# Kernel tuning notes

Hardware: AMD Instinct MI355X
Metric: run time of the kernel (lower is better)

The kernel has to match this reference:

```python
import jax, jax.numpy as jnp
import numpy as np


def setup_inputs() -> dict:
    key = jax.random.key(0)
    ks = jax.random.split(key, 9)
    B, Cin, H, W = 16, 512, 64, 64
    Cout = 256
    s_in = 0.02  # small init scale for stable softmax
    return {
        "x": jax.random.normal(ks[0], (B, Cin, H, W), dtype=jnp.float32),
        "Wq": jax.random.normal(ks[1], (Cout, Cin), dtype=jnp.float32) * s_in,
        "bq": jnp.zeros((Cout,), dtype=jnp.float32),
        "Wk": jax.random.normal(ks[2], (Cout, Cin), dtype=jnp.float32) * s_in,
        "bk": jnp.zeros((Cout,), dtype=jnp.float32),
        "Wv": jax.random.normal(ks[3], (Cout, Cin), dtype=jnp.float32) * s_in,
        "bv": jnp.zeros((Cout,), dtype=jnp.float32),
        "Wo": jax.random.normal(ks[4], (Cin, Cout), dtype=jnp.float32) * s_in,
        "bo": jnp.zeros((Cin,), dtype=jnp.float32),
    }


def reference(x, Wq, bq, Wk, bk, Wv, bv, Wo, bo):
    B, C, H, W = x.shape
    N = H * W
    xf = x.reshape(B, C, N)  # flatten spatial
    # 1x1 convs == per-pixel linear maps over channels
    q = jnp.einsum('oc,bcn->bon', Wq, xf) + bq[None, :, None]  # [B,Cout,N]
    k = jnp.einsum('oc,bcn->bon', Wk, xf) + bk[None, :, None]
    v = jnp.einsum('oc,bcn->bon', Wv, xf) + bv[None, :, None]
    # NOTE: original contracts over spatial dim N -> channel-attention [B,Cout,Cout]
    scale = jnp.asarray(N, x.dtype) ** 0.5  # query.size(-1) == N
    scores = jnp.einsum('bcn,bdn->bcd', q, k) / scale
    attn = jax.nn.softmax(scores, axis=-1)  # softmax over key-channel dim
    out = jnp.einsum('bcd,bdn->bcn', attn, v)  # [B,Cout,N]
    # permute(0,2,1).view(B,-1,H,W): row-major reshape of (B,N,Cout)
    out = jnp.transpose(out, (0, 2, 1)).reshape(B, -1, H, W)  # [B,Cout,H,W]
    out = jnp.einsum('co,bohw->bchw', Wo, out) + bo[None, :, None, None]
    return out
```

## Files before the change

### kernel.cpp

```cpp
#include <hip/hip_runtime.h>
#include <math.h>

typedef unsigned short u16;
typedef __bf16 bf16x8 __attribute__((ext_vector_type(8)));
typedef float f32x4 __attribute__((ext_vector_type(4)));
typedef unsigned short u16x4 __attribute__((ext_vector_type(4)));
typedef unsigned short u16x8 __attribute__((ext_vector_type(8)));

__device__ __forceinline__ u16 f2bf(float f) {
    unsigned int u = __float_as_uint(f);
    return (u16)((u + 0x7FFF + ((u >> 16) & 1)) >> 16);
}

#define BAR() do { __builtin_amdgcn_sched_barrier(0); __builtin_amdgcn_s_barrier(); __builtin_amdgcn_sched_barrier(0); } while (0)

__device__ __forceinline__ void stg(
    const u16* __restrict__ g, int ld, int row0, int rstride, int kt,
    u16* lds, int w, int l)
{
    #pragma unroll
    for (int qq = 0; qq < 2; ++qq) {
        const int c0 = qq * 512 + w * 64;
        const int c  = c0 + l;
        const int row = c & 255, kc = c >> 8;
        const u16* src = g + (size_t)(row0 + row * rstride) * ld + kt + kc * 8;
        __builtin_amdgcn_global_load_lds(
            (const __attribute__((address_space(1))) unsigned int*)src,
            (__attribute__((address_space(3))) unsigned int*)(lds + (size_t)c0 * 8),
            16, 0, 0);
    }
}

template<int NT>
__device__ __forceinline__ void gemm256(
    const u16* __restrict__ Ag, int ldA, int baseA, int rsA,
    const u16* __restrict__ Bg, int ldB, int n0,
    u16* sm, f32x4 (&acc)[8][4])
{
    const int tid = threadIdx.x;
    const int l = tid & 63, w = tid >> 6;
    const int p = l & 15, g = l >> 4;
    const int wm = (w >> 2) * 128;
    const int wn = (w & 3) * 64;

    #pragma unroll
    for (int t = 0; t < 3; ++t) {
        u16* buf = sm + (t & 3) * 16384;
        stg(Ag, ldA, baseA, rsA, t * 32, buf, w, l);
        stg(Bg, ldB, n0, 1, t * 32, buf + 8192, w, l);
    }

    #pragma unroll
    for (int t = 0; t < NT; ++t) {
        u16* bufA = sm + (t & 3) * 16384;
        u16* bufB = bufA + 8192;
        u16* nbuf = sm + ((t + 3) & 3) * 16384;

        if (t + 3 < NT) stg(Ag, ldA, baseA, rsA, (t + 3) * 32, nbuf, w, l);
        {
            const int r = NT - 1 - t;
            if (r >= 3)      asm volatile("s_waitcnt vmcnt(10)" ::: "memory");
            else if (r == 2) asm volatile("s_waitcnt vmcnt(8)"  ::: "memory");
            else if (r == 1) asm volatile("s_waitcnt vmcnt(4)"  ::: "memory");
            else             asm volatile("s_waitcnt vmcnt(0)"  ::: "memory");
        }
        BAR();
        bf16x8 bfr[4];
        #pragma unroll
        for (int nf = 0; nf < 4; ++nf) {
            int row = wn + nf * 16 + p;
            bfr[nf] = *(const bf16x8*)(bufB + (size_t)(g * 256 + row) * 8);
        }
        {
            bf16x8 af[4];
            #pragma unroll
            for (int i = 0; i < 4; ++i) {
                int row = wm + i * 16 + p;
                af[i] = *(const bf16x8*)(bufA + (size_t)(g * 256 + row) * 8);
            }
            __builtin_amdgcn_s_setprio(1);
            #pragma unroll
            for (int i = 0; i < 4; ++i)
                #pragma unroll
                for (int nf = 0; nf < 4; ++nf)
                    acc[i][nf] = __builtin_amdgcn_mfma_f32_16x16x32_bf16(af[i], bfr[nf], acc[i][nf], 0, 0, 0);
            __builtin_amdgcn_s_setprio(0);
        }
        if (t + 3 < NT) stg(Bg, ldB, n0, 1, (t + 3) * 32, nbuf + 8192, w, l);
        {
            bf16x8 af[4];
            #pragma unroll
            for (int i = 0; i < 4; ++i) {
                int row = wm + (4 + i) * 16 + p;
                af[i] = *(const bf16x8*)(bufA + (size_t)(g * 256 + row) * 8);
            }
            __builtin_amdgcn_s_setprio(1);
            #pragma unroll
            for (int i = 0; i < 4; ++i)
                #pragma unroll
                for (int nf = 0; nf < 4; ++nf)
                    acc[4 + i][nf] = __builtin_amdgcn_mfma_f32_16x16x32_bf16(af[i], bfr[nf], acc[4 + i][nf], 0, 0, 0);
            __builtin_amdgcn_s_setprio(0);
        }
        BAR();
    }
}

__global__ __launch_bounds__(256) void k0_prep(
    const float* __restrict__ x, u16* __restrict__ xT,
    const float* __restrict__ Wq, const float* __restrict__ Wk,
    const float* __restrict__ Wv, const float* __restrict__ Wo,
    u16* __restrict__ wqk, u16* __restrict__ wv, u16* __restrict__ wo)
{
    const int tid = threadIdx.x;
    if (blockIdx.z == 16) {
        const int bid = blockIdx.y * 64 + blockIdx.x;
        const int sel = bid >> 7;
        const int sub = bid & 127;
        const float* s = sel == 0 ? Wq : sel == 1 ? Wk : sel == 2 ? Wv : Wo;
        u16* d = sel == 0 ? wqk : sel == 1 ? (wqk + 131072) : sel == 2 ? wv : wo;
        int i = (sub * 256 + tid) * 4;
        float4 v = *(const float4*)(s + i);
        u16x4 u = {f2bf(v.x), f2bf(v.y), f2bf(v.z), f2bf(v.w)};
        *(u16x4*)(d + i) = u;
        return;
    }
    __shared__ float Tx[64 * 65];
    const int b = blockIdx.z, c0 = blockIdx.y * 64, n0 = blockIdx.x * 64;
    const float* xb = x + (size_t)b * 512 * 4096;
    #pragma unroll
    for (int r = 0; r < 4; ++r) {
        int crow = (tid >> 4) + r * 16;
        int ncol = (tid & 15) * 4;
        float4 v = *(const float4*)(xb + (size_t)(c0 + crow) * 4096 + n0 + ncol);
        Tx[(ncol + 0) * 65 + crow] = v.x;
        Tx[(ncol + 1) * 65 + crow] = v.y;
        Tx[(ncol + 2) * 65 + crow] = v.z;
        Tx[(ncol + 3) * 65 + crow] = v.w;
    }
    __syncthreads();
    u16* ob = xT + (size_t)b * 4096 * 512;
    #pragma unroll
    for (int cc = 0; cc < 2; ++cc) {
        int id = cc * 256 + tid;
        int nrow = id >> 3;
        int cch = (id & 7) * 8;
        u16x8 u;
        #pragma unroll
        for (int j = 0; j < 8; ++j) u[j] = f2bf(Tx[nrow * 65 + cch + j]);
        *(u16x8*)(ob + (size_t)(n0 + nrow) * 512 + c0 + cch) = u;
    }
}

__global__ __launch_bounds__(512, 2) void k1_qkv(
    const u16* __restrict__ wqk, const u16* __restrict__ wv,
    const float* __restrict__ bq, const float* __restrict__ bk, const float* __restrict__ bv,
    const u16* __restrict__ xT, u16* __restrict__ q, u16* __restrict__ kmat,
    u16* __restrict__ vT)
{
    __shared__ u16 sm[65536];
    const int b = blockIdx.z;
    const int y = blockIdx.y;
    const u16* xb = xT + (size_t)b * 4096 * 512;

    const int tid = threadIdx.x;
    const int l = tid & 63, w = tid >> 6;
    const int p = l & 15, g = l >> 4;
    const int wm = (w >> 2) * 128, wn = (w & 3) * 64;

    f32x4 acc[8][4] = {};

    if (y < 2) {
        const int m0 = y * 256;
        const int n0 = blockIdx.x * 256;
        gemm256<16>(wqk, 512, m0, 1, xb, 512, n0, sm, acc);

        const float* bias = (y == 0) ? bq : bk;
        u16* outp = ((y == 0) ? q : kmat) + ((size_t)b << 20);
        #pragma unroll
        for (int mf = 0; mf < 8; ++mf)
            #pragma unroll
            for (int nf = 0; nf < 4; ++nf) {
                int n = n0 + wn + nf * 16 + p;
                #pragma unroll
                for (int r = 0; r < 4; ++r) {
                    int mloc = wm + mf * 16 + g * 4 + r;
                    outp[(size_t)mloc * 4096 + n] = f2bf(acc[mf][nf][r] + bias[mloc]);
                }
            }
    } else {
        const int m0 = blockIdx.x * 256;
        gemm256<16>(xb, 512, m0, 1, wv, 512, 0, sm, acc);

        u16* outp = vT + ((size_t)b << 20);
        #pragma unroll
        for (int nf = 0; nf < 4; ++nf) {
            int d = wn + nf * 16 + p;
            float bvv = bv[d];
            #pragma unroll
            for (int mf = 0; mf < 8; ++mf) {
                #pragma unroll
                for (int r = 0; r < 4; ++r) {
                    int row = m0 + wm + mf * 16 + g * 4 + r;
                    outp[(size_t)row * 256 + d] = f2bf(acc[mf][nf][r] + bvv);
                }
            }
        }
    }
}

__global__ __launch_bounds__(512, 2) void k2_scores(
    const u16* __restrict__ q, const u16* __restrict__ kmat, float* __restrict__ spart)
{
    __shared__ u16 sm[65536];
    const int b = blockIdx.z;
    const int split = blockIdx.x;
    const u16* A = q    + ((size_t)b << 20) + split * 512;
    const u16* B = kmat + ((size_t)b << 20) + split * 512;

    f32x4 acc[8][4] = {};
    gemm256<16>(A, 4096, 0, 1, B, 4096, 0, sm, acc);

    const int tid = threadIdx.x;
    const int l = tid & 63, w = tid >> 6;
    const int p = l & 15, g = l >> 4;
    const int wm = (w >> 2) * 128, wn = (w & 3) * 64;

    float* sp = spart + ((size_t)split * 16 + b) * 65536;
    #pragma unroll
    for (int mf = 0; mf < 8; ++mf)
        #pragma unroll
        for (int nf = 0; nf < 4; ++nf) {
            int n = wn + nf * 16 + p;
            #pragma unroll
            for (int r = 0; r < 4; ++r) {
                int m = wm + mf * 16 + g * 4 + r;
                sp[(size_t)m * 256 + n] = acc[mf][nf][r] * 0.015625f;
            }
        }
}

__global__ __launch_bounds__(256) void k3_softmax(
    const float* __restrict__ sp, u16* __restrict__ attn)
{
    const int row = blockIdx.x;
    const int tid = threadIdx.x;
    const size_t STRIDE = (size_t)16 * 65536;
    const size_t base = (size_t)row * 256 + tid;

    float s = 0.f;
    #pragma unroll
    for (int i = 0; i < 8; ++i) s += sp[base + i * STRIDE];

    __shared__ float red[4];
    float m = s;
    #pragma unroll
    for (int off = 32; off >= 1; off >>= 1) m = fmaxf(m, __shfl_xor(m, off));
    if ((tid & 63) == 0) red[tid >> 6] = m;
    __syncthreads();
    m = fmaxf(fmaxf(red[0], red[1]), fmaxf(red[2], red[3]));

    float e = expf(s - m);
    float t = e;
    #pragma unroll
    for (int off = 32; off >= 1; off >>= 1) t += __shfl_xor(t, off);
    __syncthreads();
    if ((tid & 63) == 0) red[tid >> 6] = t;
    __syncthreads();
    t = red[0] + red[1] + red[2] + red[3];

    attn[base] = f2bf(e / t);
}

__global__ __launch_bounds__(512, 2) void k4_pv(
    const u16* __restrict__ attn, const u16* __restrict__ vT, u16* __restrict__ outT3)
{
    __shared__ u16 sm[65536];
    const int b  = blockIdx.z;
    const int sh = blockIdx.x;
    const u16* A = vT   + ((size_t)b << 20);
    const u16* B = attn + ((size_t)b << 16);

    f32x4 acc[8][4] = {};
    gemm256<8>(A, 256, sh, 16, B, 256, 0, sm, acc);

    const int tid = threadIdx.x;
    const int l = tid & 63, w = tid >> 6;
    const int p = l & 15, g = l >> 4;
    const int wm = (w >> 2) * 128, wn = (w & 3) * 64;

    u16* outp = outT3 + (((size_t)b * 16 + sh) << 16);
    #pragma unroll
    for (int mf = 0; mf < 8; ++mf)
        #pragma unroll
        for (int nf = 0; nf < 4; ++nf) {
            int co  = wn + nf * 16 + p;
            int nh0 = wm + mf * 16 + g * 4;
            u16x4 u = {f2bf(acc[mf][nf][0]), f2bf(acc[mf][nf][1]),
                       f2bf(acc[mf][nf][2]), f2bf(acc[mf][nf][3])};
            *(u16x4*)(outp + (size_t)co * 256 + nh0) = u;
        }
}

__global__ __launch_bounds__(512, 2) void k5_final(
    const u16* __restrict__ wo, const float* __restrict__ bo,
    const u16* __restrict__ outT3, float* __restrict__ out)
{
    __shared__ u16 sm[65536];
    const int bz = blockIdx.z;
    const int b  = bz >> 4, sh = bz & 15;
    const int m0 = blockIdx.y * 256;
    const u16* B = outT3 + ((size_t)bz << 16);

    f32x4 acc[8][4] = {};
    gemm256<8>(wo, 256, m0, 1, B, 256, 0, sm, acc);

    const int tid = threadIdx.x;
    const int l = tid & 63, w = tid >> 6;
    const int p = l & 15, g = l >> 4;
    const int wm = (w >> 2) * 128, wn = (w & 3) * 64;

    float* ob = out + (size_t)b * 2097152 + (size_t)sh * 256;
    #pragma unroll
    for (int mf = 0; mf < 8; ++mf)
        #pragma unroll
        for (int nf = 0; nf < 4; ++nf) {
            int slo = wn + nf * 16 + p;
            #pragma unroll
            for (int r = 0; r < 4; ++r) {
                int m = m0 + wm + mf * 16 + g * 4 + r;
                ob[(size_t)m * 4096 + slo] = acc[mf][nf][r] + bo[m];
            }
        }
}

extern "C" void kernel_launch(void* const* d_in, const int* in_sizes, int n_in,
                              void* d_out, int out_size, void* d_ws, size_t ws_size,
                              hipStream_t stream) {
    (void)in_sizes; (void)n_in; (void)out_size; (void)ws_size;
    const float* x  = (const float*)d_in[0];
    const float* Wq = (const float*)d_in[1];
    const float* bq = (const float*)d_in[2];
    const float* Wk = (const float*)d_in[3];
    const float* bk = (const float*)d_in[4];
    const float* Wv = (const float*)d_in[5];
    const float* bv = (const float*)d_in[6];
    const float* Wo = (const float*)d_in[7];
    const float* bo = (const float*)d_in[8];
    float* out = (float*)d_out;

    char* ws = (char*)d_ws;
    u16* xT   = (u16*)(ws + 0);
    u16* q    = (u16*)(ws + 67108864);
    u16* kmat = (u16*)(ws + 100663296);
    u16* vT   = (u16*)(ws + 134217728);
    float* spart = (float*)(ws + 0);
    u16* attn    = (u16*)(ws + 67108864);
    u16* outT3   = (u16*)(ws + 100663296);
    u16* wqk  = (u16*)(ws + 167772160);
    u16* wv   = (u16*)(ws + 168296448);
    u16* wo   = (u16*)(ws + 168558592);

    k0_prep   <<<dim3(64, 8, 17), dim3(256), 0, stream>>>(x, xT, Wq, Wk, Wv, Wo, wqk, wv, wo);
    k1_qkv    <<<dim3(16, 3, 16), dim3(512), 0, stream>>>(wqk, wv, bq, bk, bv, xT, q, kmat, vT);
    k2_scores <<<dim3(8, 1, 16),  dim3(512), 0, stream>>>(q, kmat, spart);
    k3_softmax<<<dim3(4096),      dim3(256), 0, stream>>>(spart, attn);
    k4_pv     <<<dim3(16, 1, 16), dim3(512), 0, stream>>>(attn, vT, outT3);
    k5_final  <<<dim3(1, 2, 256), dim3(512), 0, stream>>>(wo, bo, outT3, out);
}
```

Baseline: 242.1 us.

## Switch GEMM mainloop to K=64 double-buffered tiles with XOR-swizzled LDS

Result: faster. 200.3 us (-17.3%).

```diff
diff --git a/kernel.cpp b/kernel.cpp
--- a/kernel.cpp
+++ b/kernel.cpp
@@ -14,15 +14,16 @@
 
 #define BAR() do { __builtin_amdgcn_sched_barrier(0); __builtin_amdgcn_s_barrier(); __builtin_amdgcn_sched_barrier(0); } while (0)
 
-__device__ __forceinline__ void stg(
+__device__ __forceinline__ void stg64(
     const u16* __restrict__ g, int ld, int row0, int rstride, int kt,
     u16* lds, int w, int l)
 {
     #pragma unroll
-    for (int qq = 0; qq < 2; ++qq) {
+    for (int qq = 0; qq < 4; ++qq) {
         const int c0 = qq * 512 + w * 64;
         const int c  = c0 + l;
-        const int row = c & 255, kc = c >> 8;
+        const int row = c >> 3, kcs = c & 7;
+        const int kc  = kcs ^ (row & 7);
         const u16* src = g + (size_t)(row0 + row * rstride) * ld + kt + kc * 8;
         __builtin_amdgcn_global_load_lds(
             (const __attribute__((address_space(1))) unsigned int*)src,
@@ -43,63 +44,64 @@
     const int wm = (w >> 2) * 128;
     const int wn = (w & 3) * 64;
 
-    #pragma unroll
-    for (int t = 0; t < 3; ++t) {
-        u16* buf = sm + (t & 3) * 16384;
-        stg(Ag, ldA, baseA, rsA, t * 32, buf, w, l);
-        stg(Bg, ldB, n0, 1, t * 32, buf + 8192, w, l);
-    }
+    stg64(Ag, ldA, baseA, rsA, 0, sm, w, l);
+    stg64(Bg, ldB, n0, 1, 0, sm + 16384, w, l);
 
     #pragma unroll
     for (int t = 0; t < NT; ++t) {
-        u16* bufA = sm + (t & 3) * 16384;
-        u16* bufB = bufA + 8192;
-        u16* nbuf = sm + ((t + 3) & 3) * 16384;
-
-        if (t + 3 < NT) stg(Ag, ldA, baseA, rsA, (t + 3) * 32, nbuf, w, l);
+        u16* bufA = sm + (t & 1) * 32768;
+        u16* bufB = bufA + 16384;
+        u16* nbuf = sm + ((t + 1) & 1) * 32768;
+
+        if (t + 1 < NT) {
+            stg64(Ag, ldA, baseA, rsA, (t + 1) * 64, nbuf, w, l);
+            asm volatile("s_waitcnt vmcnt(4)" ::: "memory");
+        } else {
+            asm volatile("s_waitcnt vmcnt(0)" ::: "memory");
+        }
+        BAR();
+        bf16x8 bfr[4][2];
+        #pragma unroll
+        for (int nf = 0; nf < 4; ++nf) {
+            int row = wn + nf * 16 + p;
+            bfr[nf][0] = *(const bf16x8*)(bufB + (size_t)(row * 8 + ((g) ^ (row & 7))) * 8);
+            bfr[nf][1] = *(const bf16x8*)(bufB + (size_t)(row * 8 + ((4 + g) ^ (row & 7))) * 8);
+        }
         {
-            const int r = NT - 1 - t;
-            if (r >= 3)      asm volatile("s_waitcnt vmcnt(10)" ::: "memory");
-            else if (r == 2) asm volatile("s_waitcnt vmcnt(8)"  ::: "memory");
-            else if (r == 1) asm volatile("s_waitcnt vmcnt(4)"  ::: "memory");
-            else             asm volatile("s_waitcnt vmcnt(0)"  ::: "memory");
-        }
-        BAR();
-        bf16x8 bfr[4];
-        #pragma unroll
-        for (int nf = 0; nf < 4; ++nf) {
-            int row = wn + nf * 16 + p;
-            bfr[nf] = *(const bf16x8*)(bufB + (size_t)(g * 256 + row) * 8);
-        }
-        {
-            bf16x8 af[4];
+            bf16x8 af[4][2];
             #pragma unroll
             for (int i = 0; i < 4; ++i) {
                 int row = wm + i * 16 + p;
-                af[i] = *(const bf16x8*)(bufA + (size_t)(g * 256 + row) * 8);
+                af[i][0] = *(const bf16x8*)(bufA + (size_t)(row * 8 + ((g) ^ (row & 7))) * 8);
+                af[i][1] = *(const bf16x8*)(bufA + (size_t)(row * 8 + ((4 + g) ^ (row & 7))) * 8);
             }
             __builtin_amdgcn_s_setprio(1);
             #pragma unroll
             for (int i = 0; i < 4; ++i)
                 #pragma unroll
-                for (int nf = 0; nf < 4; ++nf)
-                    acc[i][nf] = __builtin_amdgcn_mfma_f32_16x16x32_bf16(af[i], bfr[nf], acc[i][nf], 0, 0, 0);
+                for (int nf = 0; nf < 4; ++nf) {
+                    acc[i][nf] = __builtin_amdgcn_mfma_f32_16x16x32_bf16(af[i][0], bfr[nf][0], acc[i][nf], 0, 0, 0);
+                    acc[i][nf] = __builtin_amdgcn_mfma_f32_16x16x32_bf16(af[i][1], bfr[nf][1], acc[i][nf], 0, 0, 0);
+                }
             __builtin_amdgcn_s_setprio(0);
         }
-        if (t + 3 < NT) stg(Bg, ldB, n0, 1, (t + 3) * 32, nbuf + 8192, w, l);
+        if (t + 1 < NT) stg64(Bg, ldB, n0, 1, (t + 1) * 64, nbuf + 16384, w, l);
         {
-            bf16x8 af[4];
+            bf16x8 af[4][2];
             #pragma unroll
             for (int i = 0; i < 4; ++i) {
                 int row = wm + (4 + i) * 16 + p;
-                af[i] = *(const bf16x8*)(bufA + (size_t)(g * 256 + row) * 8);
+                af[i][0] = *(const bf16x8*)(bufA + (size_t)(row * 8 + ((g) ^ (row & 7))) * 8);
+                af[i][1] = *(const bf16x8*)(bufA + (size_t)(row * 8 + ((4 + g) ^ (row & 7))) * 8);
             }
             __builtin_amdgcn_s_setprio(1);
             #pragma unroll
             for (int i = 0; i < 4; ++i)
                 #pragma unroll
-                for (int nf = 0; nf < 4; ++nf)
-                    acc[4 + i][nf] = __builtin_amdgcn_mfma_f32_16x16x32_bf16(af[i], bfr[nf], acc[4 + i][nf], 0, 0, 0);
+                for (int nf = 0; nf < 4; ++nf) {
+                    acc[4 + i][nf] = __builtin_amdgcn_mfma_f32_16x16x32_bf16(af[i][0], bfr[nf][0], acc[4 + i][nf], 0, 0, 0);
+                    acc[4 + i][nf] = __builtin_amdgcn_mfma_f32_16x16x32_bf16(af[i][1], bfr[nf][1], acc[4 + i][nf], 0, 0, 0);
+                }
             __builtin_amdgcn_s_setprio(0);
         }
         BAR();
@@ -161,6 +163,7 @@
     __shared__ u16 sm[65536];
     const int b = blockIdx.z;
     const int y = blockIdx.y;
+    const int tile = blockIdx.x;
     const u16* xb = xT + (size_t)b * 4096 * 512;
 
     const int tid = threadIdx.x;
@@ -172,8 +175,8 @@
 
     if (y < 2) {
         const int m0 = y * 256;
-        const int n0 = blockIdx.x * 256;
-        gemm256<16>(wqk, 512, m0, 1, xb, 512, n0, sm, acc);
+        const int n0 = tile * 256;
+        gemm256<8>(wqk, 512, m0, 1, xb, 512, n0, sm, acc);
 
         const float* bias = (y == 0) ? bq : bk;
         u16* outp = ((y == 0) ? q : kmat) + ((size_t)b << 20);
@@ -189,8 +192,8 @@
                 }
             }
     } else {
-        const int m0 = blockIdx.x * 256;
-        gemm256<16>(xb, 512, m0, 1, wv, 512, 0, sm, acc);
+        const int m0 = tile * 256;
+        gemm256<8>(xb, 512, m0, 1, wv, 512, 0, sm, acc);
 
         u16* outp = vT + ((size_t)b << 20);
         #pragma unroll
@@ -219,7 +222,7 @@
     const u16* B = kmat + ((size_t)b << 20) + split * 512;
 
     f32x4 acc[8][4] = {};
-    gemm256<16>(A, 4096, 0, 1, B, 4096, 0, sm, acc);
+    gemm256<8>(A, 4096, 0, 1, B, 4096, 0, sm, acc);
 
     const int tid = threadIdx.x;
     const int l = tid & 63, w = tid >> 6;
@@ -282,7 +285,7 @@
     const u16* B = attn + ((size_t)b << 16);
 
     f32x4 acc[8][4] = {};
-    gemm256<8>(A, 256, sh, 16, B, 256, 0, sm, acc);
+    gemm256<4>(A, 256, sh, 16, B, 256, 0, sm, acc);
 
     const int tid = threadIdx.x;
     const int l = tid & 63, w = tid >> 6;
@@ -313,7 +316,7 @@
     const u16* B = outT3 + ((size_t)bz << 16);
 
     f32x4 acc[8][4] = {};
-    gemm256<8>(wo, 256, m0, 1, B, 256, 0, sm, acc);
+    gemm256<4>(wo, 256, m0, 1, B, 256, 0, sm, acc);
 
     const int tid = threadIdx.x;
     const int l = tid & 63, w = tid >> 6;
```
